# Optimization experiments

Measured on AMD Instinct MI355X. Metric: run time of the kernel, lower is better.

The kernel has to match this reference:

```python
import jax, jax.numpy as jnp
import numpy as np

D = 256; H = 8; NL = 4; NP = 4; DH = D // H
IMG = 2048; SIDE = 256; NUM_INTERP = 2; PTS = NUM_INTERP + 1
SIDE_LENS = (32, 16, 8, 4)
LEVEL_SHAPES = ((256, 256), (128, 128), (64, 64), (32, 32))
IMG_STARTS = (0, 65536, 81920, 86016)   # level starts in full feature pyramid
VAL_STARTS = (0, 1024, 1280, 1344)      # level starts in cropped pyramid (sum=1360)


def layernorm(x, w, b, eps=1e-5):
    m = x.mean(-1, keepdims=True)
    v = ((x - m) ** 2).mean(-1, keepdims=True)
    return (x - m) * jax.lax.rsqrt(v + eps) * w + b


def pos_encode_2d(x, y, dim=128):
    # DETR-style sinusoidal 2D encoding: 64 dims for y, 64 for x, interleaved sin/cos
    half = dim // 2
    dim_t = 10000.0 ** (2.0 * (jnp.arange(half) // 2) / half)
    def enc(v):
        p = v[..., None] / dim_t
        return jnp.concatenate([jnp.sin(p[..., 0::2])[..., None],
                                jnp.cos(p[..., 1::2])[..., None]], -1).reshape(*v.shape, half)
    return jnp.concatenate([enc(y), enc(x)], -1)


def _forward(mask_flatten, tgt, query_pos, edge_coords, src_flatten, valid_ratios,
             in_proj_w, in_proj_b, out_proj_w, out_proj_b,
             norm1_w, norm1_b, norm2_w, norm2_b, norm3_w, norm3_b,
             lin0_w, lin0_b, lin1_w, lin1_b, lin2_w, lin2_b,
             off_w, off_b, attw_w, attw_b, val_w, val_b, oproj_w, oproj_b):
    E = tgt.shape[1]
    N = E * PTS
    # ---- self attention (dropout = identity, eval mode) ----
    qk = tgt + query_pos
    wq, wk, wv = jnp.split(in_proj_w, 3, 0)
    bq, bk, bv = jnp.split(in_proj_b, 3, 0)
    q = ((qk @ wq.T + bq) * (DH ** -0.5)).reshape(1, E, H, DH)
    k = (qk @ wk.T + bk).reshape(1, E, H, DH)
    v = (tgt @ wv.T + bv).reshape(1, E, H, DH)
    att = jax.nn.softmax(jnp.einsum('behd,bfhd->bhef', q, k), -1)
    sa = jnp.einsum('bhef,bfhd->behd', att, v).reshape(1, E, D) @ out_proj_w.T + out_proj_b
    x = layernorm(tgt + sa, norm2_w, norm2_b)

    # ---- geometry: interp points along edges, crop boxes, segment clipping ----
    a = edge_coords[0, :, :2]
    b = edge_coords[0, :, 2:]
    ts = jnp.arange(PTS, dtype=jnp.float32) / NUM_INTERP
    pts = (a[:, None, :] + ts[None, :, None] * (b - a)[:, None, :]).reshape(N, 2)
    ar = jnp.broadcast_to(a[:, None, :], (E, PTS, 2)).reshape(N, 2)
    br = jnp.broadcast_to(b[:, None, :], (E, PTS, 2)).reshape(N, 2)
    c = jnp.floor(pts).astype(jnp.int32)  # int() truncation, coords > 0
    cx, cy = c[:, 0], c[:, 1]
    minx = jnp.maximum(cx - SIDE // 2, 0)
    minx = jnp.where(minx + SIDE > IMG, IMG - SIDE, minx)
    miny = jnp.maximum(cy - SIDE // 2, 0)
    miny = jnp.where(miny + SIDE > IMG, IMG - SIDE, miny)
    fminx = minx.astype(jnp.float32)
    fminy = miny.astype(jnp.float32)
    d = br - ar
    def axis_clip(p0, d0, lo, hi):
        safe = jnp.where(d0 == 0, 1.0, d0)
        t1 = (lo - p0) / safe
        t2 = (hi - p0) / safe
        tlo = jnp.where(d0 == 0, 0.0, jnp.minimum(t1, t2))
        thi = jnp.where(d0 == 0, 1.0, jnp.maximum(t1, t2))
        return tlo, thi
    tlx, thx = axis_clip(ar[:, 0], d[:, 0], fminx, fminx + SIDE)
    tly, thy = axis_clip(ar[:, 1], d[:, 1], fminy, fminy + SIDE)
    t0 = jnp.maximum(jnp.maximum(tlx, tly), 0.0)
    t1 = jnp.maximum(jnp.minimum(jnp.minimum(thx, thy), 1.0), t0)
    ca = ar + t0[:, None] * d   # clipped segment first endpoint
    cb = ar + t1[:, None] * d   # clipped segment second endpoint
    pos_x = jnp.stack([ca[:, 0], cb[:, 0], cx.astype(jnp.float32)], -1)
    pos_y = jnp.stack([ca[:, 1], cb[:, 1], cy.astype(jnp.float32)], -1)
    pe = pos_encode_2d(pos_x, pos_y).reshape(N, -1)  # [N, 384]

    qfeat = jnp.broadcast_to((x + query_pos)[0][:, None, :], (E, PTS, D)).reshape(N, D)
    nq = jnp.concatenate([qfeat, pe], -1) @ lin0_w.T + lin0_b  # linear0, [N, 256]

    ref = jnp.stack([(cx.astype(jnp.float32) - fminx) / SIDE,
                     (cy.astype(jnp.float32) - fminy) / SIDE], -1)  # [N, 2]
    ref4 = ref[:, None, None, :] * valid_ratios[:, None]  # [N, 1, NL, 2]

    # ---- multi-level feature crops (gather) ----
    srcs, masks = [], []
    for l in range(NL):
        h, w = LEVEL_SHAPES[l]
        s = SIDE_LENS[l]
        ratio = IMG // w
        lx = jnp.round(fminx / ratio).astype(jnp.int32)
        ly = jnp.round(fminy / ratio).astype(jnp.int32)
        rows = ly[:, None] + jnp.arange(s)
        cols = lx[:, None] + jnp.arange(s)
        flat = (rows[:, :, None] * w + cols[:, None, :]).reshape(N, s * s)
        srcs.append(src_flatten[0, IMG_STARTS[l]:IMG_STARTS[l] + h * w][flat])
        masks.append(mask_flatten[0, IMG_STARTS[l]:IMG_STARTS[l] + h * w][flat])
    vsrc = jnp.concatenate(srcs, 1)    # [N, 1360, D]
    vmask = jnp.concatenate(masks, 1)  # [N, 1360]

    # ---- MSDeformAttn cross attention ----
    value = vsrc @ val_w.T + val_b
    value = jnp.where(vmask[..., None], 0.0, value).reshape(N, -1, H, DH)
    off = (nq @ off_w.T + off_b).reshape(N, H, NL, NP, 2)
    aw = jax.nn.softmax((nq @ attw_w.T + attw_b).reshape(N, H, NL * NP), -1).reshape(N, H, NL, NP)
    normalizer = jnp.array([[s, s] for s in SIDE_LENS], jnp.float32)  # (w, h) per crop level
    loc = ref4[:, 0, None, :, None, :] + off / normalizer[None, None, :, None, :]  # [N,H,NL,NP,2]
    n_idx = jnp.arange(N)[:, None, None]
    h_idx = jnp.arange(H)[None, :, None]
    out_acc = jnp.zeros((N, H, DH), jnp.float32)
    for l in range(NL):
        s = SIDE_LENS[l]
        vl = value[:, VAL_STARTS[l]:VAL_STARTS[l] + s * s].reshape(N, s, s, H, DH)
        g = loc[:, :, l]  # [N, H, NP, 2]
        px = g[..., 0] * s - 0.5  # grid_sample align_corners=False
        py = g[..., 1] * s - 0.5
        x0 = jnp.floor(px).astype(jnp.int32)
        y0 = jnp.floor(py).astype(jnp.int32)
        fx = px - x0
        fy = py - y0
        def tap(xi, yi):
            ok = (xi >= 0) & (xi < s) & (yi >= 0) & (yi < s)
            val = vl[n_idx, jnp.clip(yi, 0, s - 1), jnp.clip(xi, 0, s - 1), h_idx]
            return jnp.where(ok[..., None], val, 0.0)
        samp = (tap(x0, y0) * ((1 - fx) * (1 - fy))[..., None]
                + tap(x0 + 1, y0) * (fx * (1 - fy))[..., None]
                + tap(x0, y0 + 1) * ((1 - fx) * fy)[..., None]
                + tap(x0 + 1, y0 + 1) * (fx * fy)[..., None])  # [N,H,NP,DH]
        out_acc = out_acc + (aw[:, :, l, :, None] * samp).sum(2)
    ca_out = out_acc.reshape(N, D) @ oproj_w.T + oproj_b  # [N, D]

    # ---- per-edge mean pooling over interpolation samples ----
    pooled = ca_out.reshape(E, PTS, D).mean(1)[None]
    x = layernorm(x + pooled, norm1_w, norm1_b)
    # ---- FFN ----
    ffn = jax.nn.relu(x @ lin1_w.T + lin1_b) @ lin2_w.T + lin2_b
    return layernorm(x + ffn, norm3_w, norm3_b)


def setup_inputs():
    key = jax.random.key(0)
    ks = jax.random.split(key, 16)
    E = 128
    nrm = lambda k, shape, s=1.0: s * jax.random.normal(k, shape, jnp.float32)
    W = lambda k, o, i: nrm(k, (o, i), 0.02)
    theta = jax.random.uniform(ks[2], (E,), minval=0.0, maxval=2.0 * np.pi)
    start = jax.random.uniform(ks[3], (E, 2), minval=250.0, maxval=1798.0)
    end = start + 200.0 * jnp.stack([jnp.cos(theta), jnp.sin(theta)], -1)  # length 200 -> num_interp=2
    return dict(
        tgt=nrm(ks[0], (1, E, D)),
        query_pos=nrm(ks[1], (1, E, D)),
        edge_coords=jnp.concatenate([start, end], -1)[None],
        src_flatten=nrm(ks[4], (1, 87040, D)),
        mask_flatten=jnp.zeros((1, 87040), bool),
        valid_ratios=jnp.ones((1, 4, 2), jnp.float32),
        in_proj_w=W(ks[5], 3 * D, D), in_proj_b=jnp.zeros(3 * D),
        out_proj_w=W(ks[6], D, D), out_proj_b=jnp.zeros(D),
        norm1_w=jnp.ones(D), norm1_b=jnp.zeros(D),
        norm2_w=jnp.ones(D), norm2_b=jnp.zeros(D),
        norm3_w=jnp.ones(D), norm3_b=jnp.zeros(D),
        lin0_w=W(ks[7], D, 640), lin0_b=jnp.zeros(D),
        lin1_w=W(ks[8], 1024, D), lin1_b=jnp.zeros(1024),
        lin2_w=W(ks[9], D, 1024), lin2_b=jnp.zeros(D),
        off_w=W(ks[10], H * NL * NP * 2, D) * 0.1, off_b=jnp.zeros(H * NL * NP * 2),
        attw_w=W(ks[11], H * NL * NP, D), attw_b=jnp.zeros(H * NL * NP),
        val_w=W(ks[12], D, D), val_b=jnp.zeros(D),
        oproj_w=W(ks[13], D, D), oproj_b=jnp.zeros(D),
    )


def reference(tgt, query_pos, edge_coords, src_flatten, mask_flatten, valid_ratios,
              in_proj_w, in_proj_b, out_proj_w, out_proj_b,
              norm1_w, norm1_b, norm2_w, norm2_b, norm3_w, norm3_b,
              lin0_w, lin0_b, lin1_w, lin1_b, lin2_w, lin2_b,
              off_w, off_b, attw_w, attw_b, val_w, val_b, oproj_w, oproj_b):
    return _forward(mask_flatten, tgt, query_pos, edge_coords, src_flatten, valid_ratios,
                    in_proj_w, in_proj_b, out_proj_w, out_proj_b,
                    norm1_w, norm1_b, norm2_w, norm2_b, norm3_w, norm3_b,
                    lin0_w, lin0_b, lin1_w, lin1_b, lin2_w, lin2_b,
                    off_w, off_b, attw_w, attw_b, val_w, val_b, oproj_w, oproj_b)
```

## Files before the change

### kernel.cpp

```cpp
#include <hip/hip_runtime.h>
#include <math.h>


typedef unsigned int uint;

__device__ __forceinline__ float lo16(uint u) { return __uint_as_float(u << 16); }
__device__ __forceinline__ float hi16(uint u) { return __uint_as_float(u & 0xFFFF0000u); }
__device__ __forceinline__ uint bfr(float x) {
    uint u = __float_as_uint(x);
    return (u + 0x7FFFu + ((u >> 16) & 1u)) >> 16;
}

__device__ __forceinline__ float block_sum256f(float v, float* red) {
    int t = threadIdx.x;
    __syncthreads();
    #pragma unroll
    for (int off = 32; off; off >>= 1) v += __shfl_xor(v, off);
    if (t < 256 && (t & 63) == 0) red[t >> 6] = v;
    __syncthreads();
    return red[0] + red[1] + red[2] + red[3];
}

template <int K, int MI, int MO>
__device__ void gemm_unit(const float* __restrict__ IN, const float* __restrict__ IN2,
                          const float* __restrict__ W, const float* __restrict__ B,
                          float* __restrict__ OUT, int O, int OG, int u, float* smem) {
    constexpr int KC = 128;
    constexpr int LDT = KC + 4;
    float* tile = smem;
    int og = u % OG, rg = u / OG;
    int o0 = og * 8, r0 = rg * 64;
    int t = threadIdx.x;
    int r = t & 63;
    int ol = __builtin_amdgcn_readfirstlane(t >> 6);
    int oa = o0 + ol, ob = o0 + 4 + ol;
    const float* Wa = W + (size_t)oa * K;
    const float* Wb = W + (size_t)ob * K;
    float Ba = B[oa], Bb = B[ob];
    float acca = 0.f, accb = 0.f;
    for (int c = 0; c < K / KC; c++) {
        for (int idx = t; idx < 64 * KC; idx += 256) {
            int rr = idx >> 7, ii = idx & (KC - 1);
            int row = r0 + rr, col = c * KC + ii;
            float v;
            if (MI == 0) {
                v = IN[(size_t)row * K + col];
            } else {
                float tv = IN[row * 256 + col];
                v = (o0 < 512) ? tv + IN2[row * 256 + col] : tv;
            }
            tile[rr * LDT + ii] = v;
        }
        __syncthreads();
        const float4* wa4 = (const float4*)(Wa + c * KC);
        const float4* wb4 = (const float4*)(Wb + c * KC);
        const float4* trow = (const float4*)(tile + r * LDT);
        #pragma unroll
        for (int i4 = 0; i4 < KC / 4; i4++) {
            float4 x4 = trow[i4];
            float4 a4 = wa4[i4];
            float4 b4 = wb4[i4];
            acca += x4.x * a4.x; acca += x4.y * a4.y;
            acca += x4.z * a4.z; acca += x4.w * a4.w;
            accb += x4.x * b4.x; accb += x4.y * b4.y;
            accb += x4.z * b4.z; accb += x4.w * b4.w;
        }
        __syncthreads();
    }
    acca += Ba; accb += Bb;
    if (MO == 2) {
        if (oa < 256) acca *= 0.17677669529663687f;
        if (ob < 256) accb *= 0.17677669529663687f;
    }
    OUT[(size_t)(r0 + r) * O + oa] = acca;
    OUT[(size_t)(r0 + r) * O + ob] = accb;
}

__device__ void transpose_unit(const float* __restrict__ in, float* __restrict__ out,
                               int R, int C, int u, float* smem) {
    int TC = C >> 5;
    int tc = u % TC, tr = u / TC;
    int t = threadIdx.x;
    int lr = t >> 5, lc = t & 31;
    #pragma unroll
    for (int rr = 0; rr < 32; rr += 8)
        smem[(rr + lr) * 33 + lc] = in[(size_t)(tr * 32 + rr + lr) * C + tc * 32 + lc];
    __syncthreads();
    #pragma unroll
    for (int rr = 0; rr < 32; rr += 8)
        out[(size_t)(tc * 32 + rr + lr) * R + tr * 32 + lc] = smem[lc * 33 + rr + lr];
    __syncthreads();
}

__device__ void tpack_unit(const float* __restrict__ in, uint* __restrict__ P,
                           int C, int S, int F, int u, float* smem) {
    int TC = C >> 5;
    int tc = u % TC, tr = u / TC;
    int t = threadIdx.x;
    int lr = t >> 5, lc = t & 31;
    #pragma unroll
    for (int rr = 0; rr < 32; rr += 8)
        smem[(rr + lr) * 33 + lc] = in[(size_t)(tr * 32 + rr + lr) * C + tc * 32 + lc];
    __syncthreads();
    #pragma unroll
    for (int rep = 0; rep < 2; rep++) {
        int idx = rep * 256 + t;
        int c2 = idx >> 5, r = idx & 31;
        uint w0 = bfr(smem[r * 33 + 2 * c2]);
        uint w1 = bfr(smem[r * 33 + 2 * c2 + 1]);
        P[(size_t)(tc * 16 + c2) * S + F + tr * 32 + r] = (w1 << 16) | w0;
    }
    __syncthreads();
}

__global__ __launch_bounds__(256) void k_prep(const float* __restrict__ tgt,
                                              const float* __restrict__ qpos,
                                              const float* __restrict__ ipw,
                                              const float* __restrict__ ipb,
                                              const float* __restrict__ opw,
                                              const float* __restrict__ ojw,
                                              const float* __restrict__ valw,
                                              const float* __restrict__ l1w,
                                              const float* __restrict__ l2w,
                                              const float* __restrict__ l0w,
                                              const float* __restrict__ offw,
                                              const float* __restrict__ aww,
                                              float* __restrict__ qkv,
                                              float* __restrict__ opwT,
                                              float* __restrict__ ojwT,
                                              float* __restrict__ valwT,
                                              uint* __restrict__ Pl1,
                                              uint* __restrict__ Pl2,
                                              uint* __restrict__ Pl0,
                                              uint* __restrict__ Poaw) {
    __shared__ __align__(16) float smem[8448];
    int u = blockIdx.x;
    if (u < 192)       gemm_unit<256, 1, 2>(tgt, qpos, ipw, ipb, qkv, 768, 96, u, smem);
    else if (u < 256)  transpose_unit(opw, opwT, 256, 256, u - 192, smem);
    else if (u < 320)  transpose_unit(ojw, ojwT, 256, 256, u - 256, smem);
    else if (u < 384)  transpose_unit(valw, valwT, 256, 256, u - 320, smem);
    else if (u < 640)  tpack_unit(l1w, Pl1, 256, 1024, 0, u - 384, smem);
    else if (u < 896)  tpack_unit(l2w, Pl2, 1024, 256, 0, u - 640, smem);
    else if (u < 1056) tpack_unit(l0w, Pl0, 640, 256, 0, u - 896, smem);
    else if (u < 1120) tpack_unit(offw, Poaw, 256, 384, 0, u - 1056, smem);
    else               tpack_unit(aww, Poaw, 256, 384, 256, u - 1120, smem);
}

__device__ __forceinline__ void edge_geom(const float* __restrict__ ec, int e, int j,
                                          float* pxs, float* pys,
                                          float& fminx, float& fminy,
                                          float& cxf, float& cyf) {
    float ax = ec[e * 4 + 0], ay = ec[e * 4 + 1];
    float bx = ec[e * 4 + 2], by = ec[e * 4 + 3];
    float dx = bx - ax, dy = by - ay;
    float tj = 0.5f * (float)j;
    float ptx = __fadd_rn(ax, __fmul_rn(tj, dx));
    float pty = __fadd_rn(ay, __fmul_rn(tj, dy));
    cxf = floorf(ptx); cyf = floorf(pty);
    int minx = max((int)cxf - 128, 0); if (minx + 256 > 2048) minx = 2048 - 256;
    int miny = max((int)cyf - 128, 0); if (miny + 256 > 2048) miny = 2048 - 256;
    fminx = (float)minx; fminy = (float)miny;
    float tlx, thx, tly, thy;
    if (dx == 0.f) { tlx = 0.f; thx = 1.f; }
    else { float u1 = (fminx - ax) / dx, u2 = (fminx + 256.f - ax) / dx; tlx = fminf(u1, u2); thx = fmaxf(u1, u2); }
    if (dy == 0.f) { tly = 0.f; thy = 1.f; }
    else { float u1 = (fminy - ay) / dy, u2 = (fminy + 256.f - ay) / dy; tly = fminf(u1, u2); thy = fmaxf(u1, u2); }
    float t0 = fmaxf(fmaxf(tlx, tly), 0.f);
    float t1 = fmaxf(fminf(fminf(thx, thy), 1.f), t0);
    pxs[0] = __fadd_rn(ax, __fmul_rn(t0, dx)); pys[0] = __fadd_rn(ay, __fmul_rn(t0, dy));
    pxs[1] = __fadd_rn(ax, __fmul_rn(t1, dx)); pys[1] = __fadd_rn(ay, __fmul_rn(t1, dy));
    pxs[2] = cxf; pys[2] = cyf;
}

__global__ __launch_bounds__(1024) void k_edge(const float* __restrict__ qkv,
                                               const float* __restrict__ tgt,
                                               const float* __restrict__ qpos,
                                               const float* __restrict__ opwT,
                                               const float* __restrict__ opb,
                                               const float* __restrict__ n2w,
                                               const float* __restrict__ n2b,
                                               const float* __restrict__ ec,
                                               const uint* __restrict__ Pl0,
                                               const float* __restrict__ l0b,
                                               const uint* __restrict__ Poaw,
                                               const float* __restrict__ offb,
                                               const float* __restrict__ awb,
                                               const float* __restrict__ vr,
                                               const float* __restrict__ src,
                                               const unsigned char* __restrict__ mask,
                                               float* __restrict__ x1,
                                               float* __restrict__ aggb,
                                               float* __restrict__ csumb) {
    int n = blockIdx.x, t = threadIdx.x;
    int e = n / 3, j = n - e * 3;
    __shared__ __align__(16) float SH[5056];
    float* xq   = SH;
    float* sq   = SH + 256;
    float* sS   = SH + 512;
    float* wred = SH + 1536;
    float* ssum = SH + 1552;
    float* srow = SH + 1560;
    float* part = SH + 1824;
    float* red  = SH + 2848;
    float* pe      = SH + 256;
    float* nrow    = SH + 640;
    float* partial = SH + 896;
    float* offa = SH;
    float* sw   = SH + 384;
    float* uw   = SH + 896;
    float* pcs  = SH + 4992;
    __shared__ int   sg[512], rk[512], ulist[512], wtot[16], slx[8];
    __shared__ float sm[8], sinv[8], sref[2];
    if (t < 256) sq[t] = qkv[e * 768 + t];
    __syncthreads();
    int h = t >> 7;
    {
        int f = t & 127;
        const float* kf = qkv + f * 768 + 256 + h * 32;
        const float* qh = sq + h * 32;
        float s = 0.f;
        #pragma unroll 8
        for (int d = 0; d < 32; d++) s += qh[d] * kf[d];
        float m = s;
        #pragma unroll
        for (int off = 32; off; off >>= 1) m = fmaxf(m, __shfl_xor(m, off));
        if ((t & 63) == 0) wred[t >> 6] = m;
        __syncthreads();
        float hm = fmaxf(wred[2 * h], wred[2 * h + 1]);
        float ev = __expf(s - hm);
        sS[t] = ev;
        float su = ev;
        #pragma unroll
        for (int off = 32; off; off >>= 1) su += __shfl_xor(su, off);
        if ((t & 63) == 0) wred[t >> 6] = su;
        __syncthreads();
        if (t < 8) ssum[t] = 1.f / (wred[2 * t] + wred[2 * t + 1]);
    }
    {
        int o = t & 255, c = t >> 8, hh = o >> 5, d = o & 31;
        float acc = 0.f;
        #pragma unroll 8
        for (int f = c * 32; f < c * 32 + 32; f++)
            acc += sS[hh * 128 + f] * qkv[f * 768 + 512 + hh * 32 + d];
        part[t] = acc;
    }
    __syncthreads();
    if (t < 256) srow[t] = (part[t] + part[256 + t] + part[512 + t] + part[768 + t]) * ssum[t >> 5];
    __syncthreads();
    {
        int o = t & 255, c = t >> 8;
        float acc = 0.f;
        #pragma unroll 8
        for (int i = c * 64; i < c * 64 + 64; i++) acc += srow[i] * opwT[(size_t)i * 256 + o];
        part[t] = acc;
    }
    __syncthreads();
    {
        float acc = 0.f;
        if (t < 256) acc = part[t] + part[256 + t] + part[512 + t] + part[768 + t] + opb[t] + tgt[e * 256 + t];
        float mean = block_sum256f(acc, red) * (1.f / 256.f);
        float d0 = acc - mean;
        float var = block_sum256f((t < 256) ? d0 * d0 : 0.f, red) * (1.f / 256.f);
        if (t < 256) {
            float xln = d0 * rsqrtf(var + 1e-5f) * n2w[t] + n2b[t];
            if (j == 0) x1[e * 256 + t] = xln;
            xq[t] = xln + qpos[e * 256 + t];
        }
    }
    if (t < 384) {
        float pxs[3], pys[3], fmx, fmy, cxf, cyf;
        edge_geom(ec, e, j, pxs, pys, fmx, fmy, cxf, cyf);
        int jj = t >> 7, tt = t & 127, i = tt & 63, kk = i >> 1;
        float invd = __expf(-(float)kk * (9.210340371976184f / 32.f));
        float vv = (tt < 64) ? pys[jj] : pxs[jj];
        float pp = vv * invd;
        pe[t] = (i & 1) ? __cosf(pp) : __sinf(pp);
    }
    if (t == 0) {
        float pxs[3], pys[3], fmx, fmy, cxf, cyf;
        edge_geom(ec, e, j, pxs, pys, fmx, fmy, cxf, cyf);
        sref[0] = (cxf - fmx) * (1.f / 256.f);
        sref[1] = (cyf - fmy) * (1.f / 256.f);
        slx[0] = (int)rintf(fmx * 0.125f);
        slx[1] = (int)rintf(fmx * 0.0625f);
        slx[2] = (int)rintf(fmx * 0.03125f);
        slx[3] = (int)rintf(fmx * 0.015625f);
        slx[4] = (int)rintf(fmy * 0.125f);
        slx[5] = (int)rintf(fmy * 0.0625f);
        slx[6] = (int)rintf(fmy * 0.03125f);
        slx[7] = (int)rintf(fmy * 0.015625f);
    }
    __syncthreads();
    {
        int o = t & 255, kc = t >> 8;
        float acc = 0.f;
        for (int tk = 0; tk < 10; tk++) {
            const float* inb = (tk < 4) ? (xq + tk * 64) : (pe + tk * 64 - 256);
            const uint* P = Pl0 + (size_t)tk * 8192 + (size_t)(kc * 8) * 256 + o;
            #pragma unroll
            for (int kk = 0; kk < 8; kk++) {
                uint u = P[kk * 256];
                acc += inb[(kc * 8 + kk) * 2] * lo16(u);
                acc += inb[(kc * 8 + kk) * 2 + 1] * hi16(u);
            }
        }
        partial[t] = acc;
    }
    __syncthreads();
    if (t < 256) nrow[t] = partial[t] + partial[256 + t] + partial[512 + t] + partial[768 + t] + l0b[t];
    __syncthreads();
    if (t < 768) {
        int o = t % 384, kc = t / 384;
        float acc = 0.f;
        for (int tk = 0; tk < 4; tk++) {
            const float* inb = nrow + tk * 64 + kc * 32;
            const uint* P = Poaw + (size_t)tk * 12288 + (size_t)(kc * 16) * 384 + o;
            #pragma unroll
            for (int kk = 0; kk < 16; kk++) {
                uint u = P[kk * 384];
                acc += inb[kk * 2] * lo16(u);
                acc += inb[kk * 2 + 1] * hi16(u);
            }
        }
        partial[t] = acc;
    }
    __syncthreads();
    float offav = 0.f;
    if (t < 384) {
        float b = (t < 256) ? offb[t] : awb[t - 256];
        offav = partial[t] + partial[384 + t] + b;
    }
    __syncthreads();
    if (t < 384) offa[t] = offav;
    #pragma unroll
    for (int z = 0; z < 4; z++) uw[z * 1024 + t] = 0.f;
    __syncthreads();
    if (t < 8) {
        float m = -1e30f;
        for (int i = 0; i < 16; i++) m = fmaxf(m, offa[256 + t * 16 + i]);
        float s = 0.f;
        for (int i = 0; i < 16; i++) s += __expf(offa[256 + t * 16 + i] - m);
        sm[t] = m; sinv[t] = 1.f / s;
    }
    __syncthreads();
    if (t < 512) {
        int l = t >> 7, rem = t & 127;
        int hh = rem >> 4, pp = (rem >> 2) & 3, tap = t & 3;
        int s = 32 >> l, wl = 256 >> l;
        const int img_starts[4] = {0, 65536, 81920, 86016};
        float a = __expf(offa[256 + hh * 16 + l * 4 + pp] - sm[hh]) * sinv[hh];
        float slv = (float)s;
        float gx = sref[0] * vr[l * 2 + 0] + offa[hh * 32 + l * 8 + pp * 2 + 0] / slv;
        float gy = sref[1] * vr[l * 2 + 1] + offa[hh * 32 + l * 8 + pp * 2 + 1] / slv;
        float px = gx * slv - 0.5f, py = gy * slv - 0.5f;
        float x0 = floorf(px), y0 = floorf(py);
        float fx = px - x0, fy = py - y0;
        int xi = (int)x0 + (tap & 1), yi = (int)y0 + (tap >> 1);
        float wtt = ((tap & 1) ? fx : (1.f - fx)) * ((tap >> 1) ? fy : (1.f - fy));
        int g = -1;
        if (xi >= 0 && xi < s && yi >= 0 && yi < s) {
            int col = slx[l] + xi;
            int row = slx[4 + l] + yi;
            g = img_starts[l] + row * wl + col;
            if (mask[g]) g = -1;
        }
        sw[t] = a * wtt;
        sg[t] = g;
    }
    __syncthreads();
    int fi = -1;
    if (t < 512) {
        int g = sg[t];
        if (g >= 0) {
            fi = t;
            int base = t & ~127;
            for (int jj = base; jj < t; jj++) if (sg[jj] == g) { fi = jj; break; }
        }
    }
    bool islead = (fi == t);
    unsigned long long bal = __ballot(islead);
    int lane = t & 63, wid = t >> 6;
    if ((t & 63) == 0) wtot[wid] = __popcll(bal);
    __syncthreads();
    int woff = 0, U = 0;
    #pragma unroll
    for (int w = 0; w < 8; w++) {
        int c = wtot[w];
        if (w < wid) woff += c;
        U += c;
    }
    if (islead) {
        int r = woff + __popcll(bal & ((1ULL << lane) - 1ULL));
        rk[t] = r;
        ulist[r] = sg[t];
    }
    __syncthreads();
    if (fi >= 0) {
        int hh = (t >> 4) & 7;
        atomicAdd(&uw[rk[fi] * 8 + hh], sw[t]);
    }
    __syncthreads();
    {
        int ch = t & 255, q = t >> 8;
        float a0 = 0.f, a1 = 0.f;
        for (int u = 0; u < U; u++) {
            int g = ulist[u];
            float v = src[(size_t)g * 256 + ch];
            a0 += uw[u * 8 + 2 * q] * v;
            a1 += uw[u * 8 + 2 * q + 1] * v;
        }
        aggb[(size_t)n * 2048 + (2 * q) * 256 + ch] = a0;
        aggb[(size_t)n * 2048 + (2 * q + 1) * 256 + ch] = a1;
    }
    if (t < 64) {
        int hh = t >> 3, p = t & 7;
        float s = 0.f;
        for (int u = p; u < U; u += 8) s += uw[u * 8 + hh];
        pcs[t] = s;
    }
    __syncthreads();
    if (t < 8) {
        float cs = pcs[t * 8 + 0] + pcs[t * 8 + 1] + pcs[t * 8 + 2] + pcs[t * 8 + 3]
                 + pcs[t * 8 + 4] + pcs[t * 8 + 5] + pcs[t * 8 + 6] + pcs[t * 8 + 7];
        csumb[n * 8 + t] = cs;
    }
}

__global__ __launch_bounds__(1024) void k_tail(const float* __restrict__ aggb,
                                               const float* __restrict__ csumb,
                                               const float* __restrict__ x1,
                                               const float* __restrict__ valwT,
                                               const float* __restrict__ valb,
                                               const float* __restrict__ ojwT,
                                               const float* __restrict__ ojb,
                                               const float* __restrict__ n1w,
                                               const float* __restrict__ n1b,
                                               const uint* __restrict__ Pl1,
                                               const float* __restrict__ l1b,
                                               const uint* __restrict__ Pl2,
                                               const float* __restrict__ l2b,
                                               const float* __restrict__ n3w,
                                               const float* __restrict__ n3b,
                                               float* __restrict__ out) {
    int e = blockIdx.x, t = threadIdx.x;
    __shared__ float pooledA[2048], csm[8], red[8], row[256], x2s[256], h1s[1024], part[1024];
    #pragma unroll
    for (int k = 0; k < 2; k++) {
        int i = k * 1024 + t;
        pooledA[i] = (aggb[(size_t)(3 * e) * 2048 + i] + aggb[(size_t)(3 * e + 1) * 2048 + i]
                    + aggb[(size_t)(3 * e + 2) * 2048 + i]) * (1.f / 3.f);
    }
    if (t < 8)
        csm[t] = (csumb[(3 * e) * 8 + t] + csumb[(3 * e + 1) * 8 + t] + csumb[(3 * e + 2) * 8 + t]) * (1.f / 3.f);
    __syncthreads();
    {
        int o = t & 255, c = t >> 8, hh = o >> 5;
        const float* pa = pooledA + hh * 256 + c * 64;
        const float* w = valwT + (size_t)(c * 64) * 256 + o;
        float acc = 0.f;
        #pragma unroll 8
        for (int i = 0; i < 64; i++) acc += pa[i] * w[(size_t)i * 256];
        part[t] = acc;
    }
    __syncthreads();
    if (t < 256)
        row[t] = part[t] + part[256 + t] + part[512 + t] + part[768 + t] + csm[t >> 5] * valb[t];
    __syncthreads();
    {
        int o = t & 255, c = t >> 8;
        float acc = 0.f;
        #pragma unroll 8
        for (int i = c * 64; i < c * 64 + 64; i++) acc += row[i] * ojwT[(size_t)i * 256 + o];
        part[t] = acc;
    }
    __syncthreads();
    {
        float acc = 0.f;
        if (t < 256) acc = part[t] + part[256 + t] + part[512 + t] + part[768 + t] + ojb[t] + x1[e * 256 + t];
        float mean = block_sum256f(acc, red) * (1.f / 256.f);
        float d0 = acc - mean;
        float var = block_sum256f((t < 256) ? d0 * d0 : 0.f, red) * (1.f / 256.f);
        if (t < 256) x2s[t] = d0 * rsqrtf(var + 1e-5f) * n1w[t] + n1b[t];
    }
    __syncthreads();
    {
        float acc = l1b[t];
        #pragma unroll 8
        for (int k2 = 0; k2 < 128; k2++) {
            uint u = Pl1[(size_t)k2 * 1024 + t];
            acc += x2s[2 * k2] * lo16(u);
            acc += x2s[2 * k2 + 1] * hi16(u);
        }
        h1s[t] = fmaxf(acc, 0.f);
    }
    __syncthreads();
    {
        int o = t & 255, c = t >> 8;
        float acc = 0.f;
        #pragma unroll 8
        for (int k2 = c * 128; k2 < c * 128 + 128; k2++) {
            uint u = Pl2[(size_t)k2 * 256 + o];
            acc += h1s[2 * k2] * lo16(u);
            acc += h1s[2 * k2 + 1] * hi16(u);
        }
        part[t] = acc;
    }
    __syncthreads();
    {
        float acc = 0.f;
        if (t < 256) acc = part[t] + part[256 + t] + part[512 + t] + part[768 + t] + l2b[t] + x2s[t];
        float mean = block_sum256f(acc, red) * (1.f / 256.f);
        float d0 = acc - mean;
        float var = block_sum256f((t < 256) ? d0 * d0 : 0.f, red) * (1.f / 256.f);
        if (t < 256) out[e * 256 + t] = d0 * rsqrtf(var + 1e-5f) * n3w[t] + n3b[t];
    }
}

extern "C" void kernel_launch(void* const* d_in, const int* in_sizes, int n_in,
                              void* d_out, int out_size, void* d_ws, size_t ws_size,
                              hipStream_t stream) {
    (void)in_sizes; (void)n_in; (void)out_size; (void)ws_size;
    const float* tgt  = (const float*)d_in[0];
    const float* qpos = (const float*)d_in[1];
    const float* ec   = (const float*)d_in[2];
    const float* src  = (const float*)d_in[3];
    const unsigned char* mask = (const unsigned char*)d_in[4];
    const float* vr   = (const float*)d_in[5];
    const float* ipw  = (const float*)d_in[6];
    const float* ipb  = (const float*)d_in[7];
    const float* opw  = (const float*)d_in[8];
    const float* opb  = (const float*)d_in[9];
    const float* n1w  = (const float*)d_in[10];
    const float* n1b  = (const float*)d_in[11];
    const float* n2w  = (const float*)d_in[12];
    const float* n2b  = (const float*)d_in[13];
    const float* n3w  = (const float*)d_in[14];
    const float* n3b  = (const float*)d_in[15];
    const float* l0w  = (const float*)d_in[16];
    const float* l0b  = (const float*)d_in[17];
    const float* l1w  = (const float*)d_in[18];
    const float* l1b  = (const float*)d_in[19];
    const float* l2w  = (const float*)d_in[20];
    const float* l2b  = (const float*)d_in[21];
    const float* offw = (const float*)d_in[22];
    const float* offb = (const float*)d_in[23];
    const float* aww  = (const float*)d_in[24];
    const float* awb  = (const float*)d_in[25];
    const float* valw = (const float*)d_in[26];
    const float* valb = (const float*)d_in[27];
    const float* ojw  = (const float*)d_in[28];
    const float* ojb  = (const float*)d_in[29];

    float* ws     = (float*)d_ws;
    float* qkv    = ws;
    float* x1     = ws + 98304;
    float* aggb   = ws + 131072;
    float* csumb  = ws + 917504;
    float* opwT   = ws + 920576;
    float* ojwT   = ws + 986112;
    float* valwT  = ws + 1051648;
    uint*  Pl1    = (uint*)(ws + 1117184);
    uint*  Pl2    = (uint*)(ws + 1248256);
    uint*  Pl0    = (uint*)(ws + 1379328);
    uint*  Poaw   = (uint*)(ws + 1461248);

    k_prep<<<1152, 256, 0, stream>>>(tgt, qpos, ipw, ipb, opw, ojw, valw, l1w, l2w,
                                     l0w, offw, aww,
                                     qkv, opwT, ojwT, valwT, Pl1, Pl2, Pl0, Poaw);
    k_edge<<<384, 1024, 0, stream>>>(qkv, tgt, qpos, opwT, opb, n2w, n2b, ec,
                                     Pl0, l0b, Poaw, offb, awb, vr, src, mask,
                                     x1, aggb, csumb);
    k_tail<<<128, 1024, 0, stream>>>(aggb, csumb, x1, valwT, valb,
                                     ojwT, ojb, n1w, n1b, Pl1, l1b, Pl2, l2b, n3w, n3b,
                                     (float*)d_out);
}
```

Measured before the change: 265.1 us.

## Store K transposed, vectorize bf16 weight reads as uint2, unroll gather loop

```diff
diff --git a/kernel.cpp b/kernel.cpp
--- a/kernel.cpp
+++ b/kernel.cpp
@@ -24,7 +24,8 @@
 template <int K, int MI, int MO>
 __device__ void gemm_unit(const float* __restrict__ IN, const float* __restrict__ IN2,
                           const float* __restrict__ W, const float* __restrict__ B,
-                          float* __restrict__ OUT, int O, int OG, int u, float* smem) {
+                          float* __restrict__ OUT, float* __restrict__ OUT2,
+                          int O, int OG, int u, float* smem) {
     constexpr int KC = 128;
     constexpr int LDT = KC + 4;
     float* tile = smem;
@@ -71,9 +72,14 @@
     if (MO == 2) {
         if (oa < 256) acca *= 0.17677669529663687f;
         if (ob < 256) accb *= 0.17677669529663687f;
-    }
-    OUT[(size_t)(r0 + r) * O + oa] = acca;
-    OUT[(size_t)(r0 + r) * O + ob] = accb;
+        if (oa >= 256 && oa < 512) OUT2[(size_t)(oa - 256) * 128 + (r0 + r)] = acca;
+        else                       OUT[(size_t)(r0 + r) * O + oa] = acca;
+        if (ob >= 256 && ob < 512) OUT2[(size_t)(ob - 256) * 128 + (r0 + r)] = accb;
+        else                       OUT[(size_t)(r0 + r) * O + ob] = accb;
+    } else {
+        OUT[(size_t)(r0 + r) * O + oa] = acca;
+        OUT[(size_t)(r0 + r) * O + ob] = accb;
+    }
 }
 
 __device__ void transpose_unit(const float* __restrict__ in, float* __restrict__ out,
@@ -126,6 +132,7 @@
                                               const float* __restrict__ offw,
                                               const float* __restrict__ aww,
                                               float* __restrict__ qkv,
+                                              float* __restrict__ kT,
                                               float* __restrict__ opwT,
                                               float* __restrict__ ojwT,
                                               float* __restrict__ valwT,
@@ -135,7 +142,7 @@
                                               uint* __restrict__ Poaw) {
     __shared__ __align__(16) float smem[8448];
     int u = blockIdx.x;
-    if (u < 192)       gemm_unit<256, 1, 2>(tgt, qpos, ipw, ipb, qkv, 768, 96, u, smem);
+    if (u < 192)       gemm_unit<256, 1, 2>(tgt, qpos, ipw, ipb, qkv, kT, 768, 96, u, smem);
     else if (u < 256)  transpose_unit(opw, opwT, 256, 256, u - 192, smem);
     else if (u < 320)  transpose_unit(ojw, ojwT, 256, 256, u - 256, smem);
     else if (u < 384)  transpose_unit(valw, valwT, 256, 256, u - 320, smem);
@@ -173,6 +180,7 @@
 }
 
 __global__ __launch_bounds__(1024) void k_edge(const float* __restrict__ qkv,
+                                               const float* __restrict__ kT,
                                                const float* __restrict__ tgt,
                                                const float* __restrict__ qpos,
                                                const float* __restrict__ opwT,
@@ -216,11 +224,11 @@
     int h = t >> 7;
     {
         int f = t & 127;
-        const float* kf = qkv + f * 768 + 256 + h * 32;
+        const float* kf = kT + (size_t)(h * 32) * 128 + f;
         const float* qh = sq + h * 32;
         float s = 0.f;
         #pragma unroll 8
-        for (int d = 0; d < 32; d++) s += qh[d] * kf[d];
+        for (int d = 0; d < 32; d++) s += qh[d] * kf[d * 128];
         float m = s;
         #pragma unroll
         for (int off = 32; off; off >>= 1) m = fmaxf(m, __shfl_xor(m, off));
@@ -292,43 +300,49 @@
     }
     __syncthreads();
     {
-        int o = t & 255, kc = t >> 8;
-        float acc = 0.f;
-        for (int tk = 0; tk < 10; tk++) {
+        int o2 = t & 127, kc = t >> 7;
+        float acc0 = 0.f, acc1 = 0.f;
+        for (int k2g = kc * 40; k2g < kc * 40 + 40; k2g++) {
+            int tk = k2g >> 5, p = k2g & 31;
             const float* inb = (tk < 4) ? (xq + tk * 64) : (pe + tk * 64 - 256);
-            const uint* P = Pl0 + (size_t)tk * 8192 + (size_t)(kc * 8) * 256 + o;
-            #pragma unroll
-            for (int kk = 0; kk < 8; kk++) {
-                uint u = P[kk * 256];
-                acc += inb[(kc * 8 + kk) * 2] * lo16(u);
-                acc += inb[(kc * 8 + kk) * 2 + 1] * hi16(u);
-            }
-        }
-        partial[t] = acc;
-    }
-    __syncthreads();
-    if (t < 256) nrow[t] = partial[t] + partial[256 + t] + partial[512 + t] + partial[768 + t] + l0b[t];
+            float in0 = inb[2 * p], in1 = inb[2 * p + 1];
+            uint2 u2 = *(const uint2*)(Pl0 + (size_t)tk * 8192 + (size_t)p * 256 + 2 * o2);
+            acc0 += in0 * lo16(u2.x) + in1 * hi16(u2.x);
+            acc1 += in0 * lo16(u2.y) + in1 * hi16(u2.y);
+        }
+        partial[kc * 128 + o2] = acc0;
+        partial[1024 + kc * 128 + o2] = acc1;
+    }
+    __syncthreads();
+    if (t < 256) {
+        int o2 = t >> 1, sel = t & 1;
+        const float* pp = partial + sel * 1024 + o2;
+        float s = pp[0] + pp[128] + pp[256] + pp[384] + pp[512] + pp[640] + pp[768] + pp[896];
+        nrow[t] = s + l0b[t];
+    }
     __syncthreads();
     if (t < 768) {
-        int o = t % 384, kc = t / 384;
-        float acc = 0.f;
-        for (int tk = 0; tk < 4; tk++) {
-            const float* inb = nrow + tk * 64 + kc * 32;
-            const uint* P = Poaw + (size_t)tk * 12288 + (size_t)(kc * 16) * 384 + o;
-            #pragma unroll
-            for (int kk = 0; kk < 16; kk++) {
-                uint u = P[kk * 384];
-                acc += inb[kk * 2] * lo16(u);
-                acc += inb[kk * 2 + 1] * hi16(u);
-            }
-        }
-        partial[t] = acc;
+        int o2 = t % 192, kc = t / 192;
+        float acc0 = 0.f, acc1 = 0.f;
+        const float* inb = nrow + kc * 64;
+        const uint* Pb = Poaw + (size_t)kc * 12288 + 2 * o2;
+        #pragma unroll 8
+        for (int p = 0; p < 32; p++) {
+            uint2 u2 = *(const uint2*)(Pb + (size_t)p * 384);
+            float in0 = inb[2 * p], in1 = inb[2 * p + 1];
+            acc0 += in0 * lo16(u2.x) + in1 * hi16(u2.x);
+            acc1 += in0 * lo16(u2.y) + in1 * hi16(u2.y);
+        }
+        partial[kc * 192 + o2] = acc0;
+        partial[1024 + kc * 192 + o2] = acc1;
     }
     __syncthreads();
     float offav = 0.f;
     if (t < 384) {
+        int o2 = t >> 1, sel = t & 1;
+        const float* pp = partial + sel * 1024 + o2;
         float b = (t < 256) ? offb[t] : awb[t - 256];
-        offav = partial[t] + partial[384 + t] + b;
+        offav = pp[0] + pp[192] + pp[384] + pp[576] + b;
     }
     __syncthreads();
     if (t < 384) offa[t] = offav;
@@ -403,7 +417,19 @@
     {
         int ch = t & 255, q = t >> 8;
         float a0 = 0.f, a1 = 0.f;
-        for (int u = 0; u < U; u++) {
+        int u = 0;
+        for (; u + 4 <= U; u += 4) {
+            int g0 = ulist[u], g1 = ulist[u + 1], g2 = ulist[u + 2], g3 = ulist[u + 3];
+            float v0 = src[(size_t)g0 * 256 + ch];
+            float v1 = src[(size_t)g1 * 256 + ch];
+            float v2 = src[(size_t)g2 * 256 + ch];
+            float v3 = src[(size_t)g3 * 256 + ch];
+            a0 += uw[u * 8 + 2 * q] * v0;           a1 += uw[u * 8 + 2 * q + 1] * v0;
+            a0 += uw[(u + 1) * 8 + 2 * q] * v1;     a1 += uw[(u + 1) * 8 + 2 * q + 1] * v1;
+            a0 += uw[(u + 2) * 8 + 2 * q] * v2;     a1 += uw[(u + 2) * 8 + 2 * q + 1] * v2;
+            a0 += uw[(u + 3) * 8 + 2 * q] * v3;     a1 += uw[(u + 3) * 8 + 2 * q + 1] * v3;
+        }
+        for (; u < U; u++) {
             int g = ulist[u];
             float v = src[(size_t)g * 256 + ch];
             a0 += uw[u * 8 + 2 * q] * v;
@@ -484,31 +510,50 @@
     }
     __syncthreads();
     {
-        float acc = l1b[t];
-        #pragma unroll 8
-        for (int k2 = 0; k2 < 128; k2++) {
-            uint u = Pl1[(size_t)k2 * 1024 + t];
-            acc += x2s[2 * k2] * lo16(u);
-            acc += x2s[2 * k2 + 1] * hi16(u);
-        }
-        h1s[t] = fmaxf(acc, 0.f);
-    }
-    __syncthreads();
-    {
-        int o = t & 255, c = t >> 8;
+        int o2 = t & 511, kh = t >> 9;
+        float acc0 = 0.f, acc1 = 0.f;
+        const uint* Pb = Pl1 + (size_t)(kh * 64) * 1024 + 2 * o2;
+        const float* xb = x2s + kh * 128;
+        #pragma unroll 8
+        for (int p = 0; p < 64; p++) {
+            uint2 u2 = *(const uint2*)(Pb + (size_t)p * 1024);
+            float in0 = xb[2 * p], in1 = xb[2 * p + 1];
+            acc0 += in0 * lo16(u2.x) + in1 * hi16(u2.x);
+            acc1 += in0 * lo16(u2.y) + in1 * hi16(u2.y);
+        }
+        pooledA[kh * 1024 + o2] = acc0;
+        pooledA[kh * 1024 + 512 + o2] = acc1;
+    }
+    __syncthreads();
+    {
+        int o2 = t >> 1, sel = t & 1;
+        h1s[t] = fmaxf(pooledA[sel * 512 + o2] + pooledA[1024 + sel * 512 + o2] + l1b[t], 0.f);
+    }
+    __syncthreads();
+    {
+        int o2 = t & 127, c = t >> 7;
+        float acc0 = 0.f, acc1 = 0.f;
+        const uint* Pb = Pl2 + (size_t)(c * 64) * 256 + 2 * o2;
+        const float* hb = h1s + c * 128;
+        #pragma unroll 8
+        for (int p = 0; p < 64; p++) {
+            uint2 u2 = *(const uint2*)(Pb + (size_t)p * 256);
+            float in0 = hb[2 * p], in1 = hb[2 * p + 1];
+            acc0 += in0 * lo16(u2.x) + in1 * hi16(u2.x);
+            acc1 += in0 * lo16(u2.y) + in1 * hi16(u2.y);
+        }
+        pooledA[c * 128 + o2] = acc0;
+        pooledA[1024 + c * 128 + o2] = acc1;
+    }
+    __syncthreads();
+    {
         float acc = 0.f;
-        #pragma unroll 8
-        for (int k2 = c * 128; k2 < c * 128 + 128; k2++) {
-            uint u = Pl2[(size_t)k2 * 256 + o];
-            acc += h1s[2 * k2] * lo16(u);
-            acc += h1s[2 * k2 + 1] * hi16(u);
-        }
-        part[t] = acc;
-    }
-    __syncthreads();
-    {
-        float acc = 0.f;
-        if (t < 256) acc = part[t] + part[256 + t] + part[512 + t] + part[768 + t] + l2b[t] + x2s[t];
+        if (t < 256) {
+            int o2 = t >> 1, sel = t & 1;
+            const float* pp = pooledA + sel * 1024 + o2;
+            acc = pp[0] + pp[128] + pp[256] + pp[384] + pp[512] + pp[640] + pp[768] + pp[896]
+                + l2b[t] + x2s[t];
+        }
         float mean = block_sum256f(acc, red) * (1.f / 256.f);
         float d0 = acc - mean;
         float var = block_sum256f((t < 256) ? d0 * d0 : 0.f, red) * (1.f / 256.f);
@@ -563,11 +608,12 @@
     uint*  Pl2    = (uint*)(ws + 1248256);
     uint*  Pl0    = (uint*)(ws + 1379328);
     uint*  Poaw   = (uint*)(ws + 1461248);
+    float* kT     = ws + 1510400;
 
     k_prep<<<1152, 256, 0, stream>>>(tgt, qpos, ipw, ipb, opw, ojw, valw, l1w, l2w,
                                      l0w, offw, aww,
-                                     qkv, opwT, ojwT, valwT, Pl1, Pl2, Pl0, Poaw);
-    k_edge<<<384, 1024, 0, stream>>>(qkv, tgt, qpos, opwT, opb, n2w, n2b, ec,
+                                     qkv, kT, opwT, ojwT, valwT, Pl1, Pl2, Pl0, Poaw);
+    k_edge<<<384, 1024, 0, stream>>>(qkv, kT, tgt, qpos, opwT, opb, n2w, n2b, ec,
                                      Pl0, l0b, Poaw, offb, awb, vr, src, mask,
                                      x1, aggb, csumb);
     k_tail<<<128, 1024, 0, stream>>>(aggb, csumb, x1, valwT, valb,
```

New measurement: 277.5 us. +4.7%, slower.
